# Kernel optimization log

Measured on AMD Instinct MI355X. Metric: run time of the kernel, lower is better.

## Reference

```python
import jax, jax.numpy as jnp
import numpy as np

B, S, D = 2, 2048, 2048
H = 16
I = 8192  # intermediate_size
HD = I // H  # per-head intermediate dim = 512


def setup_inputs() -> dict:
    key = jax.random.key(0)
    ks = jax.random.split(key, 7)
    scale_d = 1.0 / np.sqrt(D)
    scale_i = 1.0 / np.sqrt(I)
    return {
        "x": jax.random.normal(ks[0], (B, S, D), dtype=jnp.float32),
        "adjacency": jax.random.uniform(ks[1], (B, H, S, S), dtype=jnp.float32) * (1.0 / S),
        "Wg": jax.random.normal(ks[2], (D, I), dtype=jnp.float32) * scale_d,
        "Wu": jax.random.normal(ks[3], (D, I), dtype=jnp.float32) * scale_d,
        "Wd": jax.random.normal(ks[4], (I, D), dtype=jnp.float32) * scale_i,
        "eps": jnp.zeros((H,), dtype=jnp.float32),
        "alpha": jnp.ones((H,), dtype=jnp.float32),
    }


def reference(x, adjacency, Wg, Wu, Wd, eps, alpha):
    # gate/up projections + SwiGLU: (B,S,I)
    gate = jnp.einsum("bsd,di->bsi", x, Wg)
    up = jnp.einsum("bsd,di->bsi", x, Wu)
    h_inter = jax.nn.silu(gate) * up
    # split into heads: (B,H,S,HD)
    h_heads = h_inter.reshape(B, S, H, HD).transpose(0, 2, 1, 3)
    # batched per-head GIN: (1+eps_h)*h + alpha_h * A_h @ h, all heads at once
    agg = jnp.einsum("bhst,bhtd->bhsd", adjacency, h_heads)
    e = (1.0 + eps)[None, :, None, None]
    a = alpha[None, :, None, None]
    h_gin = e * h_heads + a * agg
    # recombine heads -> (B,S,I), then down projection
    h_comb = h_gin.transpose(0, 2, 1, 3).reshape(B, S, I)
    return jnp.einsum("bsi,id->bsd", h_comb, Wd)
```

## Files before the change

kernel.cpp:

```cpp
#include <hip/hip_runtime.h>
#include <hip/hip_bf16.h>


typedef __bf16 bf16x8 __attribute__((ext_vector_type(8)));
typedef float f32x4 __attribute__((ext_vector_type(4)));

__device__ __forceinline__ unsigned short f2bf(float f) {
    union { float f; unsigned int u; } x; x.f = f;
    unsigned int r = x.u + 0x7fffu + ((x.u >> 16) & 1u);
    return (unsigned short)(r >> 16);
}
__device__ __forceinline__ float bf2f(unsigned short b) {
    union { unsigned int u; float f; } x; x.u = ((unsigned int)b) << 16;
    return x.f;
}

__device__ __forceinline__ void gload_lds16(const void* g, void* l) {
    __builtin_amdgcn_global_load_lds((const __attribute__((address_space(1))) void*)g,
                                     (__attribute__((address_space(3))) void*)l,
                                     16, 0, 0);
}


__global__ void conv_kernel(const float* __restrict__ in, unsigned short* __restrict__ out) {
    size_t i = ((size_t)blockIdx.x * 256 + threadIdx.x) * 4;
    float4 v = *(const float4*)(in + i);
    ushort4 o; o.x = f2bf(v.x); o.y = f2bf(v.y); o.z = f2bf(v.z); o.w = f2bf(v.w);
    *(ushort4*)(out + i) = o;
}

__global__ void tconv_kernel(const float* __restrict__ in, unsigned short* __restrict__ out,
                             int R, int C) {
    __shared__ float tile[64][65];
    int nbc = C >> 6;
    int bc = blockIdx.x % nbc, br = blockIdx.x / nbc;
    int r0 = br * 64, c0 = bc * 64;
    int t = threadIdx.x;
#pragma unroll
    for (int i = 0; i < 4; ++i) {
        int idx = i * 256 + t;
        int r = idx >> 4, c4 = (idx & 15) * 4;
        float4 v = *(const float4*)(in + (size_t)(r0 + r) * C + c0 + c4);
        tile[r][c4] = v.x; tile[r][c4 + 1] = v.y; tile[r][c4 + 2] = v.z; tile[r][c4 + 3] = v.w;
    }
    __syncthreads();
#pragma unroll
    for (int i = 0; i < 4; ++i) {
        int idx = i * 256 + t;
        int c = idx >> 4, r4 = (idx & 15) * 4;
        ushort4 o;
        o.x = f2bf(tile[r4][c]); o.y = f2bf(tile[r4 + 1][c]);
        o.z = f2bf(tile[r4 + 2][c]); o.w = f2bf(tile[r4 + 3][c]);
        *(ushort4*)(out + (size_t)(c0 + c) * R + r0 + r4) = o;
    }
}

template<int EPI>
__global__ void __launch_bounds__(512, 2) gemm256(
    const unsigned short* __restrict__ Ag,
    const unsigned short* __restrict__ Bg,
    const unsigned short* __restrict__ gbuf_c,
    unsigned short* __restrict__ gbuf,
    unsigned short* __restrict__ hh,
    unsigned short* __restrict__ hhT)
{
    const int K = 2048;
    __shared__ unsigned short LDS[4][16384];
    int bid = (int)blockIdx.x;
    int lb = (bid & 7) * 64 + (bid >> 3);
    int nt = lb & 31, mt = lb >> 5;
    int tid = threadIdx.x, lane = tid & 63, wave = tid >> 6;
    int wm = wave >> 2, wn = wave & 3;
    int l15 = lane & 15, l4 = lane >> 4;

    f32x4 acc[8][4] = {};

    int jl = (lane & 7) ^ (lane >> 3);
    int prow0 = wave * 16 + (lane >> 3);
    int row0 = prow0 + ((jl & 4) << 5);
    int cc = (jl & 3) << 3;
    const unsigned short* srcA0 = Ag + (size_t)(mt * 256 + row0) * K + cc;
    const unsigned short* srcA1 = srcA0 + (size_t)8 * K;
    const unsigned short* srcB0 = Bg + (size_t)(nt * 256 + row0) * K + cc;
    const unsigned short* srcB1 = srcB0 + (size_t)8 * K;

    int cA = l15 * 128 + (((l4 + wm * 4) ^ (l15 & 7)) << 4);
    int cB = ((wn & 1) * 64 + l15) * 128 + (((l4 + ((wn >> 1) << 2)) ^ (l15 & 7)) << 4);

#define STAGE_A(t_) do { char* d_ = (char*)&LDS[(t_) & 3][0] + wave * 2048;              \
        gload_lds16((const void*)(srcA0 + (size_t)(t_) * 32), (void*)d_);                \
        gload_lds16((const void*)(srcA1 + (size_t)(t_) * 32), (void*)(d_ + 1024)); } while (0)
#define STAGE_B(t_) do { char* d_ = (char*)&LDS[(t_) & 3][8192] + wave * 2048;           \
        gload_lds16((const void*)(srcB0 + (size_t)(t_) * 32), (void*)d_);                \
        gload_lds16((const void*)(srcB1 + (size_t)(t_) * 32), (void*)(d_ + 1024)); } while (0)

    STAGE_A(0); STAGE_B(0);
    STAGE_A(1); STAGE_B(1);

    for (int t = 0; t < 64; ++t) {
        if (t + 2 < 64) asm volatile("s_waitcnt vmcnt(4)" ::: "memory");
        else            asm volatile("s_waitcnt vmcnt(0)" ::: "memory");
        __builtin_amdgcn_s_barrier();
        const char* Abase = (const char*)&LDS[t & 3][0];
        const char* Bbase = Abase + 16384;
        bool more = (t + 2) < 64;
        if (more) STAGE_A(t + 2);
        bf16x8 bf[4], af[4];
#pragma unroll
        for (int ni = 0; ni < 4; ++ni) bf[ni] = *(const bf16x8*)(Bbase + cB + ni * 2048);
#pragma unroll
        for (int mi = 0; mi < 4; ++mi) af[mi] = *(const bf16x8*)(Abase + cA + mi * 2048);
        __builtin_amdgcn_s_setprio(1);
#pragma unroll
        for (int mi = 0; mi < 4; ++mi)
#pragma unroll
            for (int ni = 0; ni < 4; ++ni)
                acc[mi][ni] = __builtin_amdgcn_mfma_f32_16x16x32_bf16(af[mi], bf[ni], acc[mi][ni], 0, 0, 0);
        __builtin_amdgcn_s_setprio(0);
        if (more) STAGE_B(t + 2);
#pragma unroll
        for (int mi = 0; mi < 4; ++mi) af[mi] = *(const bf16x8*)(Abase + cA + 8192 + mi * 2048);
        __builtin_amdgcn_s_setprio(1);
#pragma unroll
        for (int mi = 0; mi < 4; ++mi)
#pragma unroll
            for (int ni = 0; ni < 4; ++ni)
                acc[4 + mi][ni] = __builtin_amdgcn_mfma_f32_16x16x32_bf16(af[mi], bf[ni], acc[4 + mi][ni], 0, 0, 0);
        __builtin_amdgcn_s_setprio(0);
    }
#undef STAGE_A
#undef STAGE_B

    if (EPI == 0) {
        ushort4* g4 = (ushort4*)gbuf;
        size_t base = ((size_t)lb * 32) * 512 + tid;
#pragma unroll
        for (int a = 0; a < 8; ++a)
#pragma unroll
            for (int ni = 0; ni < 4; ++ni) {
                f32x4 v = acc[a][ni];
                ushort4 o;
                o.x = f2bf(v[0]); o.y = f2bf(v[1]); o.z = f2bf(v[2]); o.w = f2bf(v[3]);
                g4[base + (size_t)(a * 4 + ni) * 512] = o;
            }
    } else {
        const ushort4* g4 = (const ushort4*)gbuf_c;
        size_t base = ((size_t)lb * 32) * 512 + tid;
        int rowb = mt * 256 + wm * 128 + l4 * 4;
        int colb = nt * 256 + wn * 64 + l15;
        int b = mt >> 3;
#pragma unroll
        for (int a = 0; a < 8; ++a)
#pragma unroll
            for (int ni = 0; ni < 4; ++ni) {
                ushort4 gq = g4[base + (size_t)(a * 4 + ni) * 512];
                int row = rowb + a * 16;
                int n = colb + ni * 16;
                ushort4 hv;
#pragma unroll
                for (int r = 0; r < 4; ++r) {
                    float gv = bf2f(((const unsigned short*)&gq)[r]);
                    float u = acc[a][ni][r];
                    float h = gv / (1.f + __expf(-gv)) * u;
                    unsigned short hb = f2bf(h);
                    ((unsigned short*)&hv)[r] = hb;
                    hh[(size_t)(row + r) * 8192 + n] = hb;
                }
                *(ushort4*)(hhT + ((size_t)b * 8192 + n) * 2048 + (row & 2047)) = hv;
            }
    }
}

__global__ void __launch_bounds__(512, 2) gemm_agg3(
    const float* __restrict__ adj,
    const unsigned short* __restrict__ hhT,
    const unsigned short* __restrict__ hh,
    const float* __restrict__ eps, const float* __restrict__ alpha,
    unsigned short* __restrict__ hcomb)
{
    const int S = 2048, HD = 512, I = 8192;
    __shared__ unsigned short As[2][128 * 40];
    __shared__ unsigned short Bs[2][512 * 40];
    int bid = (int)blockIdx.x;
    int lb = (bid & 7) * 64 + (bid >> 3);
    int pair = lb >> 4;
    int mt = lb & 15;
    int b = pair >> 4, h = pair & 15;
    int tid = threadIdx.x;
    int lane = tid & 63;
    int wave = tid >> 6;
    int wm = wave >> 2, wn = wave & 3;
    f32x4 acc[4][8] = {};

    const float* Ab = adj + ((size_t)pair * S + (size_t)mt * 128) * S;
    const unsigned short* Bb = hhT + ((size_t)b * I + (size_t)h * HD) * (size_t)S;

    int a_row0 = tid >> 3, a_c = (tid & 7) << 2;
    int b_row0 = tid >> 2, b_ch = (tid & 3) << 3;

    float4 pa0_0, pa1_0, pa0_1, pa1_1;
    int4 pb0_0, pb1_0, pb2_0, pb3_0, pb0_1, pb1_1, pb2_1, pb3_1;

#define AGG_LOAD(SET, K0)                                                               \
    do {                                                                                \
        pa0_##SET = *(const float4*)(Ab + (size_t)a_row0 * S + (K0) + a_c);             \
        pa1_##SET = *(const float4*)(Ab + (size_t)(a_row0 + 64) * S + (K0) + a_c);      \
        pb0_##SET = *(const int4*)(Bb + (size_t)b_row0 * S + (K0) + b_ch);              \
        pb1_##SET = *(const int4*)(Bb + (size_t)(b_row0 + 128) * S + (K0) + b_ch);      \
        pb2_##SET = *(const int4*)(Bb + (size_t)(b_row0 + 256) * S + (K0) + b_ch);      \
        pb3_##SET = *(const int4*)(Bb + (size_t)(b_row0 + 384) * S + (K0) + b_ch);      \
    } while (0)

#define AGG_WRITE(SET, BUF)                                                             \
    do {                                                                                \
        ushort4 o0, o1;                                                                 \
        o0.x = f2bf(pa0_##SET.x); o0.y = f2bf(pa0_##SET.y);                             \
        o0.z = f2bf(pa0_##SET.z); o0.w = f2bf(pa0_##SET.w);                             \
        o1.x = f2bf(pa1_##SET.x); o1.y = f2bf(pa1_##SET.y);                             \
        o1.z = f2bf(pa1_##SET.z); o1.w = f2bf(pa1_##SET.w);                             \
        *(ushort4*)((char*)As[BUF] + a_row0 * 80 + a_c * 2) = o0;                       \
        *(ushort4*)((char*)As[BUF] + (a_row0 + 64) * 80 + a_c * 2) = o1;                \
        *(int4*)((char*)Bs[BUF] + b_row0 * 80 + b_ch * 2) = pb0_##SET;                  \
        *(int4*)((char*)Bs[BUF] + (b_row0 + 128) * 80 + b_ch * 2) = pb1_##SET;          \
        *(int4*)((char*)Bs[BUF] + (b_row0 + 256) * 80 + b_ch * 2) = pb2_##SET;          \
        *(int4*)((char*)Bs[BUF] + (b_row0 + 384) * 80 + b_ch * 2) = pb3_##SET;          \
    } while (0)

    int lrow = lane & 15;
    int koff2 = ((lane >> 4) << 3) * 2;
    const char* aptr0 = (const char*)As[0] + (wm * 64 + lrow) * 80 + koff2;
    const char* bptr0 = (const char*)Bs[0] + (wn * 128 + lrow) * 80 + koff2;
    const char* aptr1 = (const char*)As[1] + (wm * 64 + lrow) * 80 + koff2;
    const char* bptr1 = (const char*)Bs[1] + (wn * 128 + lrow) * 80 + koff2;

#define AGG_COMPUTE(APTR, BPTR)                                                         \
    do {                                                                                \
        bf16x8 af[4], bfv[8];                                                           \
        _Pragma("unroll")                                                               \
        for (int mi = 0; mi < 4; ++mi) af[mi] = *(const bf16x8*)((APTR) + mi * 16 * 80);\
        _Pragma("unroll")                                                               \
        for (int ni = 0; ni < 8; ++ni) bfv[ni] = *(const bf16x8*)((BPTR) + ni * 16 * 80);\
        __builtin_amdgcn_s_setprio(1);                                                  \
        _Pragma("unroll")                                                               \
        for (int mi = 0; mi < 4; ++mi)                                                  \
            _Pragma("unroll")                                                           \
            for (int ni = 0; ni < 8; ++ni)                                              \
                acc[mi][ni] = __builtin_amdgcn_mfma_f32_16x16x32_bf16(af[mi], bfv[ni],  \
                                                                      acc[mi][ni], 0, 0, 0); \
        __builtin_amdgcn_s_setprio(0);                                                  \
    } while (0)

    AGG_LOAD(0, 0);
    AGG_WRITE(0, 0);
    AGG_LOAD(1, 32);
    asm volatile("s_waitcnt lgkmcnt(0)" ::: "memory");
    __builtin_amdgcn_s_barrier();

    for (int s = 0; s < 64; s += 2) {
        if (s + 2 < 64) AGG_LOAD(0, (s + 2) * 32);
        AGG_COMPUTE(aptr0, bptr0);
        AGG_WRITE(1, 1);
        asm volatile("s_waitcnt lgkmcnt(0)" ::: "memory");
        __builtin_amdgcn_s_barrier();
        if (s + 3 < 64) AGG_LOAD(1, (s + 3) * 32);
        AGG_COMPUTE(aptr1, bptr1);
        if (s + 2 < 64) {
            AGG_WRITE(0, 0);
            asm volatile("s_waitcnt lgkmcnt(0)" ::: "memory");
            __builtin_amdgcn_s_barrier();
        }
    }
#undef AGG_LOAD
#undef AGG_WRITE
#undef AGG_COMPUTE

    float e1 = 1.f + eps[h];
    float a1 = alpha[h];
    int s_base = mt * 128 + wm * 64;
    int d_base = wn * 128;
#pragma unroll
    for (int mi = 0; mi < 4; ++mi)
#pragma unroll
        for (int ni = 0; ni < 8; ++ni) {
            int sb = s_base + mi * 16 + ((lane >> 4) << 2);
            int d = d_base + ni * 16 + (lane & 15);
#pragma unroll
            for (int r = 0; r < 4; ++r) {
                size_t off = ((size_t)(b * S + sb + r)) * I + (size_t)h * HD + d;
                float hv = bf2f(hh[off]);
                hcomb[off] = f2bf(e1 * hv + a1 * acc[mi][ni][r]);
            }
        }
}

__global__ void __launch_bounds__(512, 2) gemm_out2(
    const unsigned short* __restrict__ hcomb,
    const unsigned short* __restrict__ WdT,
    float* __restrict__ out)
{
    const int K = 8192;
    __shared__ unsigned short LDS[4][12288];
    int bid = (int)blockIdx.x;
    int lb = (bid & 7) * 32 + (bid >> 3);
    int mt = lb >> 4, nt = lb & 15;
    int tid = threadIdx.x, lane = tid & 63, wave = tid >> 6;
    int wm = wave >> 1, wn = wave & 1;
    int l15 = lane & 15, l4 = lane >> 4;
    f32x4 acc[4][4] = {};

    int jl = (lane & 7) ^ (lane >> 3);
    int prowA = wave * 16 + (lane >> 3);
    int rowA0 = prowA + ((jl & 4) << 5);
    int ccA = (jl & 3) << 3;
    const unsigned short* srcA0 = hcomb + (size_t)(mt * 256 + rowA0) * K + ccA;
    const unsigned short* srcA1 = srcA0 + (size_t)8 * K;
    int prowB = tid >> 3;
    int jbl = (tid & 7) ^ (prowB & 7);
    int rowB0 = prowB + ((jbl & 4) << 4);
    int ccB = (jbl & 3) << 3;
    const unsigned short* srcB0 = WdT + (size_t)(nt * 128 + rowB0) * K + ccB;

    int cA0 = ((wm & 1) * 64 + l15) * 128 + (((((wm >> 1) << 2) + l4) ^ (l15 & 7)) << 4);
    int cB0 = l15 * 128 + ((((wn << 2) + l4) ^ (l15 & 7)) << 4);

#define OSTAGE(t_) do {                                                                  \
        char* dA = (char*)&LDS[(t_) & 3][0] + wave * 2048;                               \
        gload_lds16((const void*)(srcA0 + (size_t)(t_) * 32), (void*)dA);                \
        gload_lds16((const void*)(srcA1 + (size_t)(t_) * 32), (void*)(dA + 1024));       \
        char* dB = (char*)&LDS[(t_) & 3][8192] + wave * 1024;                            \
        gload_lds16((const void*)(srcB0 + (size_t)(t_) * 32), (void*)dB);                \
    } while (0)

    OSTAGE(0); OSTAGE(1);

    for (int t = 0; t < 256; ++t) {
        if (t + 2 < 256) asm volatile("s_waitcnt vmcnt(3)" ::: "memory");
        else             asm volatile("s_waitcnt vmcnt(0)" ::: "memory");
        __builtin_amdgcn_s_barrier();
        const char* Abase = (const char*)&LDS[t & 3][0];
        const char* Bbase = Abase + 16384;
        bool more = (t + 2) < 256;
        bf16x8 af[4], bf[4];
#pragma unroll
        for (int ni = 0; ni < 4; ++ni) bf[ni] = *(const bf16x8*)(Bbase + cB0 + ni * 2048);
        if (more) OSTAGE(t + 2);
#pragma unroll
        for (int mi = 0; mi < 4; ++mi) af[mi] = *(const bf16x8*)(Abase + cA0 + mi * 2048);
        __builtin_amdgcn_s_setprio(1);
#pragma unroll
        for (int mi = 0; mi < 4; ++mi)
#pragma unroll
            for (int ni = 0; ni < 4; ++ni)
                acc[mi][ni] = __builtin_amdgcn_mfma_f32_16x16x32_bf16(af[mi], bf[ni], acc[mi][ni], 0, 0, 0);
        __builtin_amdgcn_s_setprio(0);
    }
#undef OSTAGE

    int m_off = mt * 256 + wm * 64, n_off = nt * 128 + wn * 64;
#pragma unroll
    for (int mi = 0; mi < 4; ++mi)
#pragma unroll
        for (int ni = 0; ni < 4; ++ni) {
            int mbase = m_off + mi * 16 + l4 * 4;
            int n = n_off + ni * 16 + l15;
#pragma unroll
            for (int r = 0; r < 4; ++r)
                out[(size_t)(mbase + r) * 2048 + n] = acc[mi][ni][r];
        }
}

extern "C" void kernel_launch(void* const* d_in, const int* in_sizes, int n_in,
                              void* d_out, int out_size, void* d_ws, size_t ws_size,
                              hipStream_t stream) {
    const float* x     = (const float*)d_in[0];
    const float* adj   = (const float*)d_in[1];
    const float* Wg    = (const float*)d_in[2];
    const float* Wu    = (const float*)d_in[3];
    const float* Wd    = (const float*)d_in[4];
    const float* eps   = (const float*)d_in[5];
    const float* alpha = (const float*)d_in[6];
    float* out = (float*)d_out;

    unsigned short* ws    = (unsigned short*)d_ws;
    unsigned short* xb    = ws;
    unsigned short* WgT   = xb + (size_t)4096 * 2048;
    unsigned short* WuT   = WgT + (size_t)8192 * 2048;
    unsigned short* WdT   = WuT + (size_t)8192 * 2048;
    unsigned short* hh    = WdT + (size_t)2048 * 8192;
    unsigned short* hhT   = hh + (size_t)4096 * 8192;
    unsigned short* hcomb = hhT + (size_t)16384 * 2048;
    unsigned short* gbuf  = hcomb;

    conv_kernel<<<8192, 256, 0, stream>>>(x, xb);
    tconv_kernel<<<4096, 256, 0, stream>>>(Wg, WgT, 2048, 8192);
    tconv_kernel<<<4096, 256, 0, stream>>>(Wu, WuT, 2048, 8192);
    tconv_kernel<<<4096, 256, 0, stream>>>(Wd, WdT, 8192, 2048);
    gemm256<0><<<512, 512, 0, stream>>>(xb, WgT, nullptr, gbuf, nullptr, nullptr);
    gemm256<1><<<512, 512, 0, stream>>>(xb, WuT, gbuf, nullptr, hh, hhT);
    gemm_agg3<<<512, 512, 0, stream>>>(adj, hhT, hh, eps, alpha, hcomb);
    gemm_out2<<<256, 512, 0, stream>>>(hcomb, WdT, out);
}
```

Baseline: 762.7 us.

## Fold GIN self term into adjacency diagonal, drop hh buffer, deepen out-GEMM pipeline

Folds the (1+eps) self term into the aggregation GEMM by adding (1+eps)/alpha to the adjacency diagonal before the bf16 conversion. The GEMM then directly yields alpha*(A+dI)h, so the gate/up epilogue no longer writes the row-major hh copy and the aggregation epilogue no longer reads it back. The alpha==0 case falls back to reading hhT. Separately, the output GEMM's LDS ring grows from 4 to 6 stages with prefetch depth 4, which adds shared memory and may cut occupancy. Rounding the diagonal term to bf16 changes numerics slightly.

```diff
diff --git a/kernel.cpp b/kernel.cpp
--- a/kernel.cpp
+++ b/kernel.cpp
@@ -61,7 +61,6 @@
     const unsigned short* __restrict__ Bg,
     const unsigned short* __restrict__ gbuf_c,
     unsigned short* __restrict__ gbuf,
-    unsigned short* __restrict__ hh,
     unsigned short* __restrict__ hhT)
 {
     const int K = 2048;
@@ -162,9 +161,7 @@
                     float gv = bf2f(((const unsigned short*)&gq)[r]);
                     float u = acc[a][ni][r];
                     float h = gv / (1.f + __expf(-gv)) * u;
-                    unsigned short hb = f2bf(h);
-                    ((unsigned short*)&hv)[r] = hb;
-                    hh[(size_t)(row + r) * 8192 + n] = hb;
+                    ((unsigned short*)&hv)[r] = f2bf(h);
                 }
                 *(ushort4*)(hhT + ((size_t)b * 8192 + n) * 2048 + (row & 2047)) = hv;
             }
@@ -174,7 +171,6 @@
 __global__ void __launch_bounds__(512, 2) gemm_agg3(
     const float* __restrict__ adj,
     const unsigned short* __restrict__ hhT,
-    const unsigned short* __restrict__ hh,
     const float* __restrict__ eps, const float* __restrict__ alpha,
     unsigned short* __restrict__ hcomb)
 {
@@ -192,10 +188,16 @@
     int wm = wave >> 2, wn = wave & 3;
     f32x4 acc[4][8] = {};
 
+    float e1 = 1.f + eps[h];
+    float a1 = alpha[h];
+    bool a1z = (a1 == 0.f);
+    float dfac = a1z ? 0.f : (e1 / a1);
+
     const float* Ab = adj + ((size_t)pair * S + (size_t)mt * 128) * S;
     const unsigned short* Bb = hhT + ((size_t)b * I + (size_t)h * HD) * (size_t)S;
 
     int a_row0 = tid >> 3, a_c = (tid & 7) << 2;
+    int grow0 = mt * 128 + a_row0;
     int b_row0 = tid >> 2, b_ch = (tid & 3) << 3;
 
     float4 pa0_0, pa1_0, pa0_1, pa1_1;
@@ -211,8 +213,18 @@
         pb3_##SET = *(const int4*)(Bb + (size_t)(b_row0 + 384) * S + (K0) + b_ch);      \
     } while (0)
 
-#define AGG_WRITE(SET, BUF)                                                             \
+#define AGG_WRITE(SET, BUF, K0)                                                         \
     do {                                                                                \
+        int j0 = grow0 - (K0) - a_c;                                                    \
+        pa0_##SET.x += (j0 == 0) ? dfac : 0.f;                                          \
+        pa0_##SET.y += (j0 == 1) ? dfac : 0.f;                                          \
+        pa0_##SET.z += (j0 == 2) ? dfac : 0.f;                                          \
+        pa0_##SET.w += (j0 == 3) ? dfac : 0.f;                                          \
+        int j1 = j0 + 64;                                                               \
+        pa1_##SET.x += (j1 == 0) ? dfac : 0.f;                                          \
+        pa1_##SET.y += (j1 == 1) ? dfac : 0.f;                                          \
+        pa1_##SET.z += (j1 == 2) ? dfac : 0.f;                                          \
+        pa1_##SET.w += (j1 == 3) ? dfac : 0.f;                                          \
         ushort4 o0, o1;                                                                 \
         o0.x = f2bf(pa0_##SET.x); o0.y = f2bf(pa0_##SET.y);                             \
         o0.z = f2bf(pa0_##SET.z); o0.w = f2bf(pa0_##SET.w);                             \
@@ -251,7 +263,7 @@
     } while (0)
 
     AGG_LOAD(0, 0);
-    AGG_WRITE(0, 0);
+    AGG_WRITE(0, 0, 0);
     AGG_LOAD(1, 32);
     asm volatile("s_waitcnt lgkmcnt(0)" ::: "memory");
     __builtin_amdgcn_s_barrier();
@@ -259,13 +271,13 @@
     for (int s = 0; s < 64; s += 2) {
         if (s + 2 < 64) AGG_LOAD(0, (s + 2) * 32);
         AGG_COMPUTE(aptr0, bptr0);
-        AGG_WRITE(1, 1);
+        AGG_WRITE(1, 1, (s + 1) * 32);
         asm volatile("s_waitcnt lgkmcnt(0)" ::: "memory");
         __builtin_amdgcn_s_barrier();
         if (s + 3 < 64) AGG_LOAD(1, (s + 3) * 32);
         AGG_COMPUTE(aptr1, bptr1);
         if (s + 2 < 64) {
-            AGG_WRITE(0, 0);
+            AGG_WRITE(0, 0, (s + 2) * 32);
             asm volatile("s_waitcnt lgkmcnt(0)" ::: "memory");
             __builtin_amdgcn_s_barrier();
         }
@@ -274,23 +286,37 @@
 #undef AGG_WRITE
 #undef AGG_COMPUTE
 
-    float e1 = 1.f + eps[h];
-    float a1 = alpha[h];
     int s_base = mt * 128 + wm * 64;
     int d_base = wn * 128;
-#pragma unroll
-    for (int mi = 0; mi < 4; ++mi)
-#pragma unroll
-        for (int ni = 0; ni < 8; ++ni) {
-            int sb = s_base + mi * 16 + ((lane >> 4) << 2);
-            int d = d_base + ni * 16 + (lane & 15);
-#pragma unroll
-            for (int r = 0; r < 4; ++r) {
-                size_t off = ((size_t)(b * S + sb + r)) * I + (size_t)h * HD + d;
-                float hv = bf2f(hh[off]);
-                hcomb[off] = f2bf(e1 * hv + a1 * acc[mi][ni][r]);
+    if (!a1z) {
+#pragma unroll
+        for (int mi = 0; mi < 4; ++mi)
+#pragma unroll
+            for (int ni = 0; ni < 8; ++ni) {
+                int sb = s_base + mi * 16 + ((lane >> 4) << 2);
+                int d = d_base + ni * 16 + (lane & 15);
+#pragma unroll
+                for (int r = 0; r < 4; ++r) {
+                    size_t off = ((size_t)(b * S + sb + r)) * I + (size_t)h * HD + d;
+                    hcomb[off] = f2bf(a1 * acc[mi][ni][r]);
+                }
             }
-        }
+    } else {
+#pragma unroll
+        for (int mi = 0; mi < 4; ++mi)
+#pragma unroll
+            for (int ni = 0; ni < 8; ++ni) {
+                int sb = s_base + mi * 16 + ((lane >> 4) << 2);
+                int d = d_base + ni * 16 + (lane & 15);
+                size_t col = (size_t)h * HD + d;
+                ushort4 hq = *(const ushort4*)(hhT + ((size_t)b * I + col) * S + sb);
+#pragma unroll
+                for (int r = 0; r < 4; ++r) {
+                    size_t off = ((size_t)(b * S + sb + r)) * I + col;
+                    hcomb[off] = f2bf(e1 * bf2f(((const unsigned short*)&hq)[r]));
+                }
+            }
+    }
 }
 
 __global__ void __launch_bounds__(512, 2) gemm_out2(
@@ -299,7 +325,7 @@
     float* __restrict__ out)
 {
     const int K = 8192;
-    __shared__ unsigned short LDS[4][12288];
+    __shared__ unsigned short LDS[6][12288];
     int bid = (int)blockIdx.x;
     int lb = (bid & 7) * 32 + (bid >> 3);
     int mt = lb >> 4, nt = lb & 15;
@@ -324,26 +350,28 @@
     int cB0 = l15 * 128 + ((((wn << 2) + l4) ^ (l15 & 7)) << 4);
 
 #define OSTAGE(t_) do {                                                                  \
-        char* dA = (char*)&LDS[(t_) & 3][0] + wave * 2048;                               \
+        char* dA = (char*)&LDS[(t_) % 6][0] + wave * 2048;                               \
         gload_lds16((const void*)(srcA0 + (size_t)(t_) * 32), (void*)dA);                \
         gload_lds16((const void*)(srcA1 + (size_t)(t_) * 32), (void*)(dA + 1024));       \
-        char* dB = (char*)&LDS[(t_) & 3][8192] + wave * 1024;                            \
+        char* dB = (char*)&LDS[(t_) % 6][8192] + wave * 1024;                            \
         gload_lds16((const void*)(srcB0 + (size_t)(t_) * 32), (void*)dB);                \
     } while (0)
 
-    OSTAGE(0); OSTAGE(1);
+    OSTAGE(0); OSTAGE(1); OSTAGE(2); OSTAGE(3);
 
     for (int t = 0; t < 256; ++t) {
-        if (t + 2 < 256) asm volatile("s_waitcnt vmcnt(3)" ::: "memory");
-        else             asm volatile("s_waitcnt vmcnt(0)" ::: "memory");
+        if (t + 3 < 256)      asm volatile("s_waitcnt vmcnt(9)" ::: "memory");
+        else if (t + 2 < 256) asm volatile("s_waitcnt vmcnt(6)" ::: "memory");
+        else if (t + 1 < 256) asm volatile("s_waitcnt vmcnt(3)" ::: "memory");
+        else                  asm volatile("s_waitcnt vmcnt(0)" ::: "memory");
         __builtin_amdgcn_s_barrier();
-        const char* Abase = (const char*)&LDS[t & 3][0];
+        const char* Abase = (const char*)&LDS[t % 6][0];
         const char* Bbase = Abase + 16384;
-        bool more = (t + 2) < 256;
+        bool more = (t + 4) < 256;
         bf16x8 af[4], bf[4];
 #pragma unroll
         for (int ni = 0; ni < 4; ++ni) bf[ni] = *(const bf16x8*)(Bbase + cB0 + ni * 2048);
-        if (more) OSTAGE(t + 2);
+        if (more) OSTAGE(t + 4);
 #pragma unroll
         for (int mi = 0; mi < 4; ++mi) af[mi] = *(const bf16x8*)(Abase + cA0 + mi * 2048);
         __builtin_amdgcn_s_setprio(1);
@@ -386,8 +414,7 @@
     unsigned short* WgT   = xb + (size_t)4096 * 2048;
     unsigned short* WuT   = WgT + (size_t)8192 * 2048;
     unsigned short* WdT   = WuT + (size_t)8192 * 2048;
-    unsigned short* hh    = WdT + (size_t)2048 * 8192;
-    unsigned short* hhT   = hh + (size_t)4096 * 8192;
+    unsigned short* hhT   = WdT + (size_t)2048 * 8192;
     unsigned short* hcomb = hhT + (size_t)16384 * 2048;
     unsigned short* gbuf  = hcomb;
 
@@ -395,8 +422,8 @@
     tconv_kernel<<<4096, 256, 0, stream>>>(Wg, WgT, 2048, 8192);
     tconv_kernel<<<4096, 256, 0, stream>>>(Wu, WuT, 2048, 8192);
     tconv_kernel<<<4096, 256, 0, stream>>>(Wd, WdT, 8192, 2048);
-    gemm256<0><<<512, 512, 0, stream>>>(xb, WgT, nullptr, gbuf, nullptr, nullptr);
-    gemm256<1><<<512, 512, 0, stream>>>(xb, WuT, gbuf, nullptr, hh, hhT);
-    gemm_agg3<<<512, 512, 0, stream>>>(adj, hhT, hh, eps, alpha, hcomb);
+    gemm256<0><<<512, 512, 0, stream>>>(xb, WgT, nullptr, gbuf, nullptr);
+    gemm256<1><<<512, 512, 0, stream>>>(xb, WuT, gbuf, nullptr, hhT);
+    gemm_agg3<<<512, 512, 0, stream>>>(adj, hhT, eps, alpha, hcomb);
     gemm_out2<<<256, 512, 0, stream>>>(hcomb, WdT, out);
 }
```

After: 719.1 us. 1.06x faster.
